# Performance work log

Measured on AMD Instinct MI355X. Metric: run time of the kernel, lower is better.

## Reference

```python
import jax, jax.numpy as jnp
import numpy as np

BANDS, ROWS, SIM_THRESH = 16, 8, 0.5


def setup_inputs() -> dict:
    key = jax.random.key(0)
    k1, k2 = jax.random.split(key)
    N, D = 8192, 256
    Z = jax.random.normal(k1, (N, D), dtype=jnp.float32)
    # random hyperplanes ~ N(0, I), (bands*rows, D) -- sampled once (torch samples in forward)
    planes = jax.random.normal(k2, (BANDS * ROWS, D), dtype=jnp.float32)
    return {"Z": Z, "planes": planes}


def reference(Z, planes):
    N, D = Z.shape
    # signature: sign of projections, (bands, rows, N); +/-1 vs bool is equivalent for bucketing
    sig_bits = (planes @ Z.T >= 0).reshape(BANDS, ROWS, N)
    # bit-pack each band's row-signature into an integer key == hashing the signature bytes
    bit_weights = (2 ** jnp.arange(ROWS)).astype(jnp.int32)
    keys = jnp.einsum('brn,r->bn', sig_bits.astype(jnp.int32), bit_weights)  # (bands, N)
    # cosine pairwise similarity (row-normalized GEMM)
    Zn = Z / jnp.linalg.norm(Z, axis=1, keepdims=True)
    sim = Zn @ Zn.T  # (N, N)
    # number of bands in which i and j fall in the same LSH bucket
    def band_match(acc, k):
        return acc + (k[:, None] == k[None, :]).astype(jnp.float32), None
    counts, _ = jax.lax.scan(band_match, jnp.zeros((N, N), jnp.float32), keys)
    # original masks the diagonal with -inf, thresholds at sim_thresh, and emits one
    # (sim) entry per matching band into an uncoalesced sparse tensor; densified this
    # is counts * sim on surviving off-diagonal pairs.
    mask = (sim >= SIM_THRESH) & (~jnp.eye(N, dtype=bool))
    return jnp.where(mask, counts * sim, 0.0)
```

## Files before the change

### kernel.cpp

```cpp
#include <hip/hip_runtime.h>

typedef __attribute__((ext_vector_type(8))) short short8;
typedef __attribute__((ext_vector_type(4))) float floatx4;

#define N_PTS 8192
#define D_DIM 256
#define N_PLANES 128

__device__ inline unsigned short f2bf(float f) {
    unsigned int x = __float_as_uint(f);
    unsigned int r = (x + 0x7fffu + ((x >> 16) & 1u)) >> 16;
    return (unsigned short)r;
}

__device__ inline int zbytes(unsigned int w) {
    unsigned int t = ((w & 0x7f7f7f7fu) + 0x7f7f7f7fu) | w | 0x7f7f7f7fu;
    return __popc(~t);
}

__device__ inline void load_lds16(const unsigned short* g, unsigned short* l) {
    __builtin_amdgcn_global_load_lds(
        (const __attribute__((address_space(1))) unsigned int*)g,
        (__attribute__((address_space(3))) unsigned int*)l, 16, 0, 0);
}

__global__ void norm_kernel(const float* __restrict__ Z,
                            unsigned short* __restrict__ Zn) {
    int n = blockIdx.x;
    int lane = threadIdx.x;
    const float4* zr = (const float4*)(Z + (size_t)n * D_DIM);
    float4 v = zr[lane];
    float ss = v.x * v.x + v.y * v.y + v.z * v.z + v.w * v.w;
#pragma unroll
    for (int off = 32; off > 0; off >>= 1) ss += __shfl_down(ss, off);
    ss = __shfl(ss, 0);
    float inv = rsqrtf(ss);
    ushort4 o;
    o.x = f2bf(v.x * inv);
    o.y = f2bf(v.y * inv);
    o.z = f2bf(v.z * inv);
    o.w = f2bf(v.w * inv);
    ((ushort4*)(Zn + (size_t)n * D_DIM))[lane] = o;
}

__global__ __launch_bounds__(256) void keys_kernel(
    const float* __restrict__ Z, const float* __restrict__ planes,
    unsigned int* __restrict__ keys4) {
    __shared__ __align__(16) float zs[32][D_DIM];
    int t = threadIdx.x;
    int base = blockIdx.x * 32;

    const float4* zsrc = (const float4*)(Z + (size_t)base * D_DIM);
    float4* zdst = (float4*)&zs[0][0];
#pragma unroll
    for (int i = 0; i < 8; ++i) zdst[t + i * 256] = zsrc[t + i * 256];
    __syncthreads();

    int p = t & 127;
    int hf = t >> 7;
    int wave = t >> 6, lane = t & 63;
    const float4* pr = (const float4*)(planes + (size_t)p * D_DIM);

    float acc[16] = {};
    for (int kk = 0; kk < D_DIM / 4; ++kk) {
        float4 pv = pr[kk];
#pragma unroll
        for (int j = 0; j < 16; ++j) {
            float4 zv = *(const float4*)&zs[hf * 16 + j][kk * 4];
            acc[j] += pv.x * zv.x + pv.y * zv.y + pv.z * zv.z + pv.w * zv.w;
        }
    }

#pragma unroll
    for (int j = 0; j < 16; ++j) {
        unsigned long long mask = __ballot(acc[j] >= 0.0f);
        if (lane < 2) {
            keys4[(size_t)(base + hf * 16 + j) * 4 + (wave & 1) * 2 + lane] =
                (unsigned int)(mask >> (32 * lane));
        }
    }
}

__global__ __launch_bounds__(256) void gemm_kernel(
    const unsigned short* __restrict__ Zn, const uint4* __restrict__ keys,
    float* __restrict__ out) {
    __shared__ __align__(16) unsigned short As[1024 * 8];
    __shared__ __align__(16) unsigned short Bs[1024 * 8];
    __shared__ uint4 krow[128];
    __shared__ uint4 kcol[128];

    int t = threadIdx.x;
    int rowBase = blockIdx.y * 128;
    int colBase = blockIdx.x * 128;
    if (t < 128)
        krow[t] = keys[rowBase + t];
    else
        kcol[t - 128] = keys[colBase + (t - 128)];

    int wave = t >> 6, lane = t & 63;
    int wm = wave >> 1, wn = wave & 1;
    int quad = lane >> 4, l16 = lane & 15;

    floatx4 acc[4][4] = {};

    for (int s = 0; s < 4; ++s) {
        __syncthreads();
#pragma unroll
        for (int i = 0; i < 4; ++i) {
            int sa = i * 256 + t;
            int c = sa >> 7, row = sa & 127;
            size_t gOff = (size_t)row * D_DIM + s * 64 + c * 8;
            load_lds16(Zn + (size_t)rowBase * D_DIM + gOff, &As[sa * 8]);
            load_lds16(Zn + (size_t)colBase * D_DIM + gOff, &Bs[sa * 8]);
        }
        __syncthreads();

#pragma unroll
        for (int k2 = 0; k2 < 2; ++k2) {
            int cb = k2 * 4 + quad;
            short8 afr[4], bfr[4];
#pragma unroll
            for (int mt = 0; mt < 4; ++mt)
                afr[mt] = *(const short8*)&As[(cb * 128 + wm * 64 + mt * 16 + l16) * 8];
#pragma unroll
            for (int nt = 0; nt < 4; ++nt)
                bfr[nt] = *(const short8*)&Bs[(cb * 128 + wn * 64 + nt * 16 + l16) * 8];
#pragma unroll
            for (int mt = 0; mt < 4; ++mt)
#pragma unroll
                for (int nt = 0; nt < 4; ++nt)
                    acc[mt][nt] = __builtin_amdgcn_mfma_f32_16x16x32_bf16(
                        afr[mt], bfr[nt], acc[mt][nt], 0, 0, 0);
        }
    }

#pragma unroll
    for (int mt = 0; mt < 4; ++mt) {
        int liBase = wm * 64 + mt * 16 + quad * 4;
#pragma unroll
        for (int nt = 0; nt < 4; ++nt) {
            int lj = wn * 64 + nt * 16 + l16;
            int gj = colBase + lj;
            uint4 kj = kcol[lj];
#pragma unroll
            for (int r = 0; r < 4; ++r) {
                int li = liBase + r;
                int gi = rowBase + li;
                float s = acc[mt][nt][r];
                float v = 0.0f;
                if (s >= 0.5f && gi != gj) {
                    uint4 ki = krow[li];
                    int c = zbytes(ki.x ^ kj.x) + zbytes(ki.y ^ kj.y) +
                            zbytes(ki.z ^ kj.z) + zbytes(ki.w ^ kj.w);
                    v = s * (float)c;
                }
                out[(size_t)gi * N_PTS + gj] = v;
            }
        }
    }
}

extern "C" void kernel_launch(void* const* d_in, const int* in_sizes, int n_in,
                              void* d_out, int out_size, void* d_ws,
                              size_t ws_size, hipStream_t stream) {
    const float* Z = (const float*)d_in[0];
    const float* planes = (const float*)d_in[1];
    float* out = (float*)d_out;

    unsigned short* Zn = (unsigned short*)d_ws;
    unsigned int* keys4 =
        (unsigned int*)((char*)d_ws + (size_t)N_PTS * D_DIM * 2);

    norm_kernel<<<N_PTS, 64, 0, stream>>>(Z, Zn);
    keys_kernel<<<N_PTS / 32, 256, 0, stream>>>(Z, planes, keys4);
    gemm_kernel<<<dim3(N_PTS / 128, N_PTS / 128), 256, 0, stream>>>(
        Zn, (const uint4*)keys4, out);
}
```

Baseline: 341.2 us.

## Exploit similarity symmetry by computing upper-triangular tiles and mirroring through LDS

Launches only the upper-triangular 128x128 output tiles, recovering tile coordinates from a linear block index. Each off-diagonal tile writes its result directly and also writes the transpose, staged through a padded per-wave LDS buffer that reuses the GEMM operand space. This roughly halves the MFMA and operand-load work, since the similarity and band-match count are symmetric. In exchange, the mirrored stores are less coalesced (16-float segments per row) and each block carries extra LDS traffic and index arithmetic.

```diff
diff --git a/kernel.cpp b/kernel.cpp
--- a/kernel.cpp
+++ b/kernel.cpp
@@ -6,6 +6,7 @@
 #define N_PTS 8192
 #define D_DIM 256
 #define N_PLANES 128
+#define NTILE 64
 
 __device__ inline unsigned short f2bf(float f) {
     unsigned int x = __float_as_uint(f);
@@ -89,9 +90,16 @@
     __shared__ uint4 krow[128];
     __shared__ uint4 kcol[128];
 
+    int idx = blockIdx.x;
+    int bi = (int)((129.0f - sqrtf(16641.0f - 8.0f * (float)idx)) * 0.5f);
+    while ((bi + 1) * NTILE - ((bi + 1) * bi) / 2 <= idx) ++bi;
+    while (bi * NTILE - (bi * (bi - 1)) / 2 > idx) --bi;
+    int bj = bi + (idx - (bi * NTILE - (bi * (bi - 1)) / 2));
+    int rowBase = bi * 128;
+    int colBase = bj * 128;
+    bool diag = (bi == bj);
+
     int t = threadIdx.x;
-    int rowBase = blockIdx.y * 128;
-    int colBase = blockIdx.x * 128;
     if (t < 128)
         krow[t] = keys[rowBase + t];
     else
@@ -134,27 +142,42 @@
         }
     }
 
+    __syncthreads();
+
+    float* Tt = (wave < 2) ? (float*)(As + wave * 2176)
+                           : (float*)(Bs + (wave - 2) * 2176);
+
 #pragma unroll
     for (int mt = 0; mt < 4; ++mt) {
-        int liBase = wm * 64 + mt * 16 + quad * 4;
 #pragma unroll
         for (int nt = 0; nt < 4; ++nt) {
-            int lj = wn * 64 + nt * 16 + l16;
-            int gj = colBase + lj;
-            uint4 kj = kcol[lj];
+            int ljL = nt * 16 + l16;
+            int gj = colBase + wn * 64 + ljL;
+            uint4 kj = kcol[wn * 64 + ljL];
 #pragma unroll
             for (int r = 0; r < 4; ++r) {
-                int li = liBase + r;
-                int gi = rowBase + li;
+                int liL = mt * 16 + quad * 4 + r;
+                int gi = rowBase + wm * 64 + liL;
                 float s = acc[mt][nt][r];
                 float v = 0.0f;
                 if (s >= 0.5f && gi != gj) {
-                    uint4 ki = krow[li];
+                    uint4 ki = krow[wm * 64 + liL];
                     int c = zbytes(ki.x ^ kj.x) + zbytes(ki.y ^ kj.y) +
                             zbytes(ki.z ^ kj.z) + zbytes(ki.w ^ kj.w);
                     v = s * (float)c;
                 }
                 out[(size_t)gi * N_PTS + gj] = v;
+                Tt[ljL * 17 + (quad * 4 + r)] = v;
+            }
+        }
+        if (!diag) {
+            size_t mBase = (size_t)(colBase + wn * 64) * N_PTS + rowBase +
+                           wm * 64 + mt * 16 + l16;
+#pragma unroll
+            for (int it = 0; it < 16; ++it) {
+                int gjL = it * 4 + quad;
+                float v = Tt[gjL * 17 + l16];
+                out[mBase + (size_t)gjL * N_PTS] = v;
             }
         }
     }
@@ -173,6 +196,6 @@
 
     norm_kernel<<<N_PTS, 64, 0, stream>>>(Z, Zn);
     keys_kernel<<<N_PTS / 32, 256, 0, stream>>>(Z, planes, keys4);
-    gemm_kernel<<<dim3(N_PTS / 128, N_PTS / 128), 256, 0, stream>>>(
-        Zn, (const uint4*)keys4, out);
-}
+    int nblocks = NTILE * (NTILE + 1) / 2;
+    gemm_kernel<<<nblocks, 256, 0, stream>>>(Zn, (const uint4*)keys4, out);
+}
```

Result: no change. 346.8 us (+1.6%).
